# Performance work log

Measured on AMD Instinct MI355X. Metric: run time of the kernel, lower is better.

Reference implementation:

```python
import jax, jax.numpy as jnp
import numpy as np

B, LQ, LK, D = 8, 2048, 2048, 1024


def setup_inputs() -> dict:
    key = jax.random.key(0)
    k1, k2, k3, k4, k5 = jax.random.split(key, 5)
    inp = jax.random.normal(k1, (B, LQ, D), dtype=jnp.float32)
    memory = jax.random.normal(k2, (B, LK, D), dtype=jnp.float32)
    # 0/1 float mask over memory positions (1 = masked out)
    mask = (jax.random.uniform(k3, (B, LK)) < 0.15).astype(jnp.float32)
    # nn.Linear(D, 1, bias=False): weight shape [1, D], kaiming-uniform-ish init
    w_input = jax.random.uniform(k4, (1, D), dtype=jnp.float32,
                                 minval=-1.0 / np.sqrt(D), maxval=1.0 / np.sqrt(D))
    # dot_scale ~ U(0, 1/sqrt(D)) per original .uniform_(1/input_size**0.5)
    dot_scale = jax.random.uniform(k5, (D,), dtype=jnp.float32,
                                   minval=0.0, maxval=1.0 / np.sqrt(D))
    return {"input": inp, "memory": memory, "mask": mask,
            "w_input": w_input, "dot_scale": dot_scale}


def reference(input, memory, mask, w_input, dot_scale):
    # input_dot: Linear(D,1,bias=False) -> [B, Lq, 1]
    input_dot = jnp.einsum('bqd,od->bqo', input, w_input)  # o == 1
    # cross_dot: (input * dot_scale) @ memory^T -> [B, Lq, Lk]
    cross_dot = jnp.einsum('bqd,bkd->bqk', input * dot_scale, memory)
    att = input_dot + cross_dot - 1e30 * mask[:, None, :]
    weight_one = jax.nn.softmax(att, axis=-1)  # [B, Lq, Lk]
    output_one = jnp.einsum('bqk,bkd->bqd', weight_one, memory)
    return output_one
```

## Files before the change

### kernel.cpp

```cpp
#include <hip/hip_runtime.h>

#define B_  8
#define LQ_ 2048
#define LK_ 2048
#define D_  1024

typedef unsigned short u16;
using short8  = __attribute__((ext_vector_type(8))) short;
using floatx4 = __attribute__((ext_vector_type(4))) float;

#define GAS __attribute__((address_space(1)))
#define LAS __attribute__((address_space(3)))

__device__ __forceinline__ u16 f2bf(float f) {
  unsigned u = __float_as_uint(f);
  u += 0x7fffu + ((u >> 16) & 1u);
  return (u16)(u >> 16);
}
__device__ __forceinline__ float bf2f(u16 h) {
  return __uint_as_float(((unsigned)h) << 16);
}

__global__ void prep(const float* __restrict__ in, const float* __restrict__ mem,
                     const float* __restrict__ ds, u16* __restrict__ qb,
                     u16* __restrict__ mb, u16* __restrict__ mbT,
                     float* __restrict__ denom) {
  __shared__ u16 tile[64][68];
  int tid = threadIdx.x;
  int tx = tid & 15, ty = tid >> 4;
  int b = blockIdx.z;

  if (denom && blockIdx.y == 16 && blockIdx.x == 0 && blockIdx.z == 0) {
    float4 z = {0.f, 0.f, 0.f, 0.f};
    float4* d4 = (float4*)denom;
#pragma unroll
    for (int i = 0; i < (B_ * LQ_ / 4) / 256; i++)
      d4[tid + i * 256] = z;
  }

  if (blockIdx.y < 16) {
    int k0 = blockIdx.x * 64, d0 = blockIdx.y * 64;
    const float* mB = mem + (size_t)b * LK_ * D_;
    u16* mbB = mb  + (size_t)b * LK_ * D_;
    u16* mtB = mbT + (size_t)b * D_ * LK_;
#pragma unroll
    for (int i = 0; i < 4; i++) {
      int r = ty + 16 * i;
      float4 v = *(const float4*)(mB + (size_t)(k0 + r) * D_ + d0 + tx * 4);
      ushort4 h;
      h.x = f2bf(v.x); h.y = f2bf(v.y); h.z = f2bf(v.z); h.w = f2bf(v.w);
      *(ushort4*)(mbB + (size_t)(k0 + r) * D_ + d0 + tx * 4) = h;
      *(ushort4*)(&tile[r][tx * 4]) = h;
    }
    __syncthreads();
#pragma unroll
    for (int i = 0; i < 4; i++) {
      int rr = ty + 16 * i;
      ushort4 o;
      o.x = tile[tx * 4 + 0][rr];
      o.y = tile[tx * 4 + 1][rr];
      o.z = tile[tx * 4 + 2][rr];
      o.w = tile[tx * 4 + 3][rr];
      *(ushort4*)(mtB + (size_t)(d0 + rr) * LK_ + k0 + tx * 4) = o;
    }
  } else {
    int q0 = blockIdx.x * 64, d0 = (blockIdx.y - 16) * 64;
    const float* iB = in + (size_t)b * LQ_ * D_;
    u16* qB = qb + (size_t)b * LQ_ * D_;
    float4 s4 = *(const float4*)(ds + d0 + tx * 4);
#pragma unroll
    for (int i = 0; i < 4; i++) {
      int r = ty + 16 * i;
      float4 v = *(const float4*)(iB + (size_t)(q0 + r) * D_ + d0 + tx * 4);
      ushort4 h;
      h.x = f2bf(v.x * s4.x); h.y = f2bf(v.y * s4.y);
      h.z = f2bf(v.z * s4.z); h.w = f2bf(v.w * s4.w);
      *(ushort4*)(qB + (size_t)(q0 + r) * D_ + d0 + tx * 4) = h;
    }
  }
}

template <int MODE>
__global__ __launch_bounds__(512, 2) void gemm_bt(
    const u16* __restrict__ A, const u16* __restrict__ Bm,
    void* __restrict__ C, const float* __restrict__ mask,
    float* __restrict__ denom, int K, int ld, int ldc,
    size_t sA, size_t sB, size_t sC) {
  __shared__ __align__(16) u16 As[2 * 16384];
  __shared__ __align__(16) u16 Bs[2 * 16384];

  const int tid = threadIdx.x;
  const int lane = tid & 63, w = tid >> 6;
  const int lm = lane & 15, quad = (lane >> 4) & 3;
  const int wm = (w >> 2) * 128, wn = (w & 3) * 64;

  const int tiles_n = gridDim.x;
  int bid = (blockIdx.z * gridDim.y + blockIdx.y) * tiles_n + blockIdx.x;
  int bz = bid & 7;
  int s = bid >> 3;
  const int GM = 4;
  int per_group = GM * tiles_n;
  int group = s / per_group;
  int rem = s - group * per_group;
  int tm = group * GM + (rem & (GM - 1));
  int tn = rem >> 2;

  const u16* Ab = A  + (size_t)bz * sA + (size_t)(tm * 256) * ld;
  const u16* Bb = Bm + (size_t)bz * sB + (size_t)(tn * 256) * ld;

  int goff[4], lofs[4];
#pragma unroll
  for (int j = 0; j < 4; j++) {
    int c = tid + 512 * j;
    int rho = c >> 3, sl = c & 7;
    goff[j] = rho * ld + (sl ^ (rho & 7)) * 8;
    lofs[j] = c * 8;
  }

  auto stage = [&](int buf, int k0) {
#pragma unroll
    for (int j = 0; j < 4; j++)
      __builtin_amdgcn_global_load_lds((GAS void*)(Ab + goff[j] + k0),
                                       (LAS void*)(As + buf * 16384 + lofs[j]),
                                       16, 0, 0);
#pragma unroll
    for (int j = 0; j < 4; j++)
      __builtin_amdgcn_global_load_lds((GAS void*)(Bb + goff[j] + k0),
                                       (LAS void*)(Bs + buf * 16384 + lofs[j]),
                                       16, 0, 0);
  };

  const int ka0 = (((0 + quad)) ^ (lm & 7)) * 8;
  const int ka1 = (((4 + quad)) ^ (lm & 7)) * 8;

  short8 bf[8], afE[4], afO[4];
  floatx4 acc[8][4];
#pragma unroll
  for (int i = 0; i < 8; i++)
#pragma unroll
    for (int j = 0; j < 4; j++)
      acc[i][j] = {0.f, 0.f, 0.f, 0.f};
  float rs[8] = {0.f, 0.f, 0.f, 0.f, 0.f, 0.f, 0.f, 0.f};

#define SB __builtin_amdgcn_sched_barrier(0)
#define LG(N) { asm volatile("s_waitcnt lgkmcnt(" #N ")" ::: "memory"); SB; }
#define VM0   { asm volatile("s_waitcnt vmcnt(0)" ::: "memory"); SB; }

#define RD_BF(CO)                                                             \
  { _Pragma("unroll")                                                         \
    for (int n = 0; n < 4; n++) {                                             \
      bf[n * 2 + 0] = *(const short8*)(Bs + (CO) + ((wn + n * 16 + lm) << 6) + ka0); \
      bf[n * 2 + 1] = *(const short8*)(Bs + (CO) + ((wn + n * 16 + lm) << 6) + ka1); \
    } }
#define RD_AF(BANK, MP, CO)                                                   \
  { _Pragma("unroll")                                                         \
    for (int mi = 0; mi < 2; mi++) {                                          \
      BANK[mi * 2 + 0] = *(const short8*)(As + (CO) + ((wm + (MP) * 32 + mi * 16 + lm) << 6) + ka0); \
      BANK[mi * 2 + 1] = *(const short8*)(As + (CO) + ((wm + (MP) * 32 + mi * 16 + lm) << 6) + ka1); \
    } }
#define SUMS(BANK, P)                                                         \
  if constexpr (MODE == 2) {                                                  \
    _Pragma("unroll")                                                         \
    for (int mi = 0; mi < 2; mi++)                                            \
      _Pragma("unroll")                                                       \
      for (int ks = 0; ks < 2; ks++) {                                        \
        uint4 u = *(const uint4*)&BANK[mi * 2 + ks];                          \
        rs[(P) * 2 + mi] +=                                                   \
            __uint_as_float(u.x << 16) + __uint_as_float(u.x & 0xffff0000u)   \
          + __uint_as_float(u.y << 16) + __uint_as_float(u.y & 0xffff0000u)   \
          + __uint_as_float(u.z << 16) + __uint_as_float(u.z & 0xffff0000u)   \
          + __uint_as_float(u.w << 16) + __uint_as_float(u.w & 0xffff0000u);  \
      } }
#define MM(P, BANK)                                                           \
  { __builtin_amdgcn_s_setprio(1);                                            \
    _Pragma("unroll")                                                         \
    for (int mi = 0; mi < 2; mi++)                                            \
      _Pragma("unroll")                                                       \
      for (int n = 0; n < 4; n++)                                             \
        _Pragma("unroll")                                                     \
        for (int ks = 0; ks < 2; ks++)                                        \
          acc[(P) * 2 + mi][n] = __builtin_amdgcn_mfma_f32_16x16x32_bf16(     \
              BANK[mi * 2 + ks], bf[n * 2 + ks], acc[(P) * 2 + mi][n], 0, 0, 0); \
    __builtin_amdgcn_s_setprio(0); }

  const int NT = K >> 6;
  stage(0, 0);
  VM0;
  __builtin_amdgcn_s_barrier();

  for (int t = 0; t < NT; ++t) {
    const int co = (t & 1) * 16384;
    const int nbuf = (t & 1) ^ 1;
    const bool have = (t + 1 < NT);
    const int kn = (t + 1) << 6;

    SB;
    RD_BF(co) RD_AF(afE, 0, co) RD_AF(afO, 1, co) SB;
    if (have) stage(nbuf, kn);
    SB;
    LG(4)  SUMS(afE, 0) MM(0, afE) SB;
    RD_AF(afE, 2, co) SB;
    LG(4)  SUMS(afO, 1) MM(1, afO) SB;
    RD_AF(afO, 3, co) SB;
    LG(4)  SUMS(afE, 2) MM(2, afE) SB;
    LG(0)  SUMS(afO, 3) MM(3, afO) SB;
    VM0;
    __builtin_amdgcn_s_barrier();
  }
#undef MM
#undef SUMS
#undef RD_AF
#undef RD_BF
#undef LG
#undef VM0
#undef SB

  const int gm0 = tm * 256 + wm + quad * 4;
  const int gn0 = tn * 256 + wn + lm;
  const size_t cb = (size_t)bz * sC;

  if constexpr (MODE == 1) {
    const float* mrow = mask + (size_t)bz * LK_;
    bool msk[4];
#pragma unroll
    for (int ni = 0; ni < 4; ni++) msk[ni] = (mrow[gn0 + ni * 16] != 0.0f);
#pragma unroll
    for (int mi = 0; mi < 8; mi++) {
#pragma unroll
      for (int r = 0; r < 4; r++) {
        int row = gm0 + mi * 16 + r;
        size_t rowoff = cb + (size_t)row * ldc + gn0;
        float part = 0.f;
#pragma unroll
        for (int ni = 0; ni < 4; ni++) {
          float e = msk[ni] ? 0.f : __expf(acc[mi][ni][r]);
          u16 h = f2bf(e);
          ((u16*)C)[rowoff + ni * 16] = h;
          part += bf2f(h);
        }
        if (denom) {
          part += __shfl_xor(part, 1, 64);
          part += __shfl_xor(part, 2, 64);
          part += __shfl_xor(part, 4, 64);
          part += __shfl_xor(part, 8, 64);
          if (lm == 0) atomicAdd(&denom[(size_t)bz * LQ_ + row], part);
        }
      }
    }
  } else if constexpr (MODE == 0) {
#pragma unroll
    for (int mi = 0; mi < 8; mi++) {
#pragma unroll
      for (int r = 0; r < 4; r++) {
        int row = gm0 + mi * 16 + r;
        float is = 1.0f / denom[(size_t)bz * LQ_ + row];
        size_t rowoff = cb + (size_t)row * ldc + gn0;
#pragma unroll
        for (int ni = 0; ni < 4; ni++)
          ((float*)C)[rowoff + ni * 16] = acc[mi][ni][r] * is;
      }
    }
  } else {
    float inv[8];
#pragma unroll
    for (int mi = 0; mi < 8; mi++) {
      rs[mi] += __shfl_xor(rs[mi], 16, 64);
      rs[mi] += __shfl_xor(rs[mi], 32, 64);
      inv[mi] = 1.0f / rs[mi];
    }
#pragma unroll
    for (int mi = 0; mi < 8; mi++) {
#pragma unroll
      for (int r = 0; r < 4; r++) {
        size_t rowoff = cb + (size_t)(gm0 + mi * 16 + r) * ldc + gn0;
        float is = __shfl(inv[mi], quad * 4 + r, 64);
#pragma unroll
        for (int ni = 0; ni < 4; ni++)
          ((float*)C)[rowoff + ni * 16] = acc[mi][ni][r] * is;
      }
    }
  }
}

extern "C" void kernel_launch(void* const* d_in, const int* in_sizes, int n_in,
                              void* d_out, int out_size, void* d_ws, size_t ws_size,
                              hipStream_t stream) {
  const float* input  = (const float*)d_in[0];
  const float* memory = (const float*)d_in[1];
  const float* mask   = (const float*)d_in[2];
  const float* dscale = (const float*)d_in[4];

  char* ws = (char*)d_ws;
  u16* qb  = (u16*)(ws);
  u16* mb  = (u16*)(ws + (size_t)32 * 1024 * 1024);
  u16* mbT = (u16*)(ws + (size_t)64 * 1024 * 1024);
  u16* E   = (u16*)(ws + (size_t)96 * 1024 * 1024);
  size_t base = (size_t)160 * 1024 * 1024;
  bool have_denom = ws_size >= base + (size_t)B_ * LQ_ * sizeof(float);
  float* denom = have_denom ? (float*)(ws + base) : nullptr;
  float* out = (float*)d_out;

  hipLaunchKernelGGL(prep, dim3(32, 32, B_), dim3(256), 0, stream,
                     input, memory, dscale, qb, mb, mbT, denom);
  hipLaunchKernelGGL((gemm_bt<1>), dim3(LK_ / 256, LQ_ / 256, B_), dim3(512), 0,
                     stream, qb, mb, (void*)E, mask, denom, D_, D_, LK_,
                     (size_t)LQ_ * D_, (size_t)LK_ * D_, (size_t)LQ_ * LK_);
  if (have_denom)
    hipLaunchKernelGGL((gemm_bt<0>), dim3(D_ / 256, LQ_ / 256, B_), dim3(512), 0,
                       stream, E, mbT, (void*)out, nullptr, denom, LK_, LK_, D_,
                       (size_t)LQ_ * LK_, (size_t)D_ * LK_, (size_t)LQ_ * D_);
  else
    hipLaunchKernelGGL((gemm_bt<2>), dim3(D_ / 256, LQ_ / 256, B_), dim3(512), 0,
                       stream, E, mbT, (void*)out, nullptr, nullptr, LK_, LK_, D_,
                       (size_t)LQ_ * LK_, (size_t)D_ * LK_, (size_t)LQ_ * D_);
}
```

Before: 314.1 us.

## Shrink GEMM tiles to 256x128 with BK=32 and 256-thread blocks

Reworks the shared bf16 GEMM kernel to use 256x128 output tiles, a K-step of 32 and 4 waves of 256 threads instead of 256x256 tiles, K-step 64 and 8 waves. The LDS swizzle changes to a 4-slot XOR pattern. The finely interleaved LDS-read/MFMA schedule is replaced by one full fragment load, a single lgkmcnt(0) wait, then all MFMAs. This doubles the grid, lowers LDS use per block for more occupancy, and simplifies scheduling. In exchange it halves B-tile reuse, doubles the number of K iterations and barriers, and loses the overlap of LDS reads with MFMA work.

```diff
diff --git a/kernel.cpp b/kernel.cpp
--- a/kernel.cpp
+++ b/kernel.cpp
@@ -81,18 +81,18 @@
 }
 
 template <int MODE>
-__global__ __launch_bounds__(512, 2) void gemm_bt(
+__global__ __launch_bounds__(256, 2) void gemm_bt(
     const u16* __restrict__ A, const u16* __restrict__ Bm,
     void* __restrict__ C, const float* __restrict__ mask,
     float* __restrict__ denom, int K, int ld, int ldc,
     size_t sA, size_t sB, size_t sC) {
-  __shared__ __align__(16) u16 As[2 * 16384];
-  __shared__ __align__(16) u16 Bs[2 * 16384];
+  __shared__ __align__(16) u16 As[2 * 8192];
+  __shared__ __align__(16) u16 Bs[2 * 4096];
 
   const int tid = threadIdx.x;
   const int lane = tid & 63, w = tid >> 6;
   const int lm = lane & 15, quad = (lane >> 4) & 3;
-  const int wm = (w >> 2) * 128, wn = (w & 3) * 64;
+  const int wm = (w >> 1) * 128, wn = (w & 1) * 64;
 
   const int tiles_n = gridDim.x;
   int bid = (blockIdx.z * gridDim.y + blockIdx.y) * tiles_n + blockIdx.x;
@@ -106,34 +106,38 @@
   int tn = rem >> 2;
 
   const u16* Ab = A  + (size_t)bz * sA + (size_t)(tm * 256) * ld;
-  const u16* Bb = Bm + (size_t)bz * sB + (size_t)(tn * 256) * ld;
-
-  int goff[4], lofs[4];
+  const u16* Bb = Bm + (size_t)bz * sB + (size_t)(tn * 128) * ld;
+
+  int goffA[4], goffB[2];
 #pragma unroll
   for (int j = 0; j < 4; j++) {
-    int c = tid + 512 * j;
-    int rho = c >> 3, sl = c & 7;
-    goff[j] = rho * ld + (sl ^ (rho & 7)) * 8;
-    lofs[j] = c * 8;
+    int c = tid + 256 * j;
+    int rho = c >> 2, sl = c & 3;
+    goffA[j] = rho * ld + (sl ^ (rho & 3)) * 8;
+  }
+#pragma unroll
+  for (int j = 0; j < 2; j++) {
+    int c = tid + 256 * j;
+    int rho = c >> 2, sl = c & 3;
+    goffB[j] = rho * ld + (sl ^ (rho & 3)) * 8;
   }
 
   auto stage = [&](int buf, int k0) {
 #pragma unroll
     for (int j = 0; j < 4; j++)
-      __builtin_amdgcn_global_load_lds((GAS void*)(Ab + goff[j] + k0),
-                                       (LAS void*)(As + buf * 16384 + lofs[j]),
-                                       16, 0, 0);
-#pragma unroll
-    for (int j = 0; j < 4; j++)
-      __builtin_amdgcn_global_load_lds((GAS void*)(Bb + goff[j] + k0),
-                                       (LAS void*)(Bs + buf * 16384 + lofs[j]),
-                                       16, 0, 0);
+      __builtin_amdgcn_global_load_lds(
+          (GAS void*)(Ab + goffA[j] + k0),
+          (LAS void*)(As + buf * 8192 + (tid + 256 * j) * 8), 16, 0, 0);
+#pragma unroll
+    for (int j = 0; j < 2; j++)
+      __builtin_amdgcn_global_load_lds(
+          (GAS void*)(Bb + goffB[j] + k0),
+          (LAS void*)(Bs + buf * 4096 + (tid + 256 * j) * 8), 16, 0, 0);
   };
 
-  const int ka0 = (((0 + quad)) ^ (lm & 7)) * 8;
-  const int ka1 = (((4 + quad)) ^ (lm & 7)) * 8;
-
-  short8 bf[8], afE[4], afO[4];
+  const int ka = (quad ^ (lm & 3)) * 8;
+
+  short8 af[8], bf[4];
   floatx4 acc[8][4];
 #pragma unroll
   for (int i = 0; i < 8; i++)
@@ -143,80 +147,58 @@
   float rs[8] = {0.f, 0.f, 0.f, 0.f, 0.f, 0.f, 0.f, 0.f};
 
 #define SB __builtin_amdgcn_sched_barrier(0)
-#define LG(N) { asm volatile("s_waitcnt lgkmcnt(" #N ")" ::: "memory"); SB; }
-#define VM0   { asm volatile("s_waitcnt vmcnt(0)" ::: "memory"); SB; }
-
-#define RD_BF(CO)                                                             \
-  { _Pragma("unroll")                                                         \
-    for (int n = 0; n < 4; n++) {                                             \
-      bf[n * 2 + 0] = *(const short8*)(Bs + (CO) + ((wn + n * 16 + lm) << 6) + ka0); \
-      bf[n * 2 + 1] = *(const short8*)(Bs + (CO) + ((wn + n * 16 + lm) << 6) + ka1); \
-    } }
-#define RD_AF(BANK, MP, CO)                                                   \
-  { _Pragma("unroll")                                                         \
-    for (int mi = 0; mi < 2; mi++) {                                          \
-      BANK[mi * 2 + 0] = *(const short8*)(As + (CO) + ((wm + (MP) * 32 + mi * 16 + lm) << 6) + ka0); \
-      BANK[mi * 2 + 1] = *(const short8*)(As + (CO) + ((wm + (MP) * 32 + mi * 16 + lm) << 6) + ka1); \
-    } }
-#define SUMS(BANK, P)                                                         \
-  if constexpr (MODE == 2) {                                                  \
-    _Pragma("unroll")                                                         \
-    for (int mi = 0; mi < 2; mi++)                                            \
-      _Pragma("unroll")                                                       \
-      for (int ks = 0; ks < 2; ks++) {                                        \
-        uint4 u = *(const uint4*)&BANK[mi * 2 + ks];                          \
-        rs[(P) * 2 + mi] +=                                                   \
-            __uint_as_float(u.x << 16) + __uint_as_float(u.x & 0xffff0000u)   \
-          + __uint_as_float(u.y << 16) + __uint_as_float(u.y & 0xffff0000u)   \
-          + __uint_as_float(u.z << 16) + __uint_as_float(u.z & 0xffff0000u)   \
-          + __uint_as_float(u.w << 16) + __uint_as_float(u.w & 0xffff0000u);  \
-      } }
-#define MM(P, BANK)                                                           \
-  { __builtin_amdgcn_s_setprio(1);                                            \
-    _Pragma("unroll")                                                         \
-    for (int mi = 0; mi < 2; mi++)                                            \
-      _Pragma("unroll")                                                       \
-      for (int n = 0; n < 4; n++)                                             \
-        _Pragma("unroll")                                                     \
-        for (int ks = 0; ks < 2; ks++)                                        \
-          acc[(P) * 2 + mi][n] = __builtin_amdgcn_mfma_f32_16x16x32_bf16(     \
-              BANK[mi * 2 + ks], bf[n * 2 + ks], acc[(P) * 2 + mi][n], 0, 0, 0); \
-    __builtin_amdgcn_s_setprio(0); }
-
-  const int NT = K >> 6;
+#define LG0 { asm volatile("s_waitcnt lgkmcnt(0)" ::: "memory"); SB; }
+#define VM0 { asm volatile("s_waitcnt vmcnt(0)" ::: "memory"); SB; }
+
+  const int NT = K >> 5;
   stage(0, 0);
   VM0;
   __builtin_amdgcn_s_barrier();
 
   for (int t = 0; t < NT; ++t) {
-    const int co = (t & 1) * 16384;
+    const int ca = (t & 1) * 8192;
+    const int cbf = (t & 1) * 4096;
     const int nbuf = (t & 1) ^ 1;
     const bool have = (t + 1 < NT);
-    const int kn = (t + 1) << 6;
+    const int kn = (t + 1) << 5;
 
     SB;
-    RD_BF(co) RD_AF(afE, 0, co) RD_AF(afO, 1, co) SB;
+#pragma unroll
+    for (int n = 0; n < 4; n++)
+      bf[n] = *(const short8*)(Bs + cbf + ((wn + n * 16 + lm) << 5) + ka);
+#pragma unroll
+    for (int m = 0; m < 8; m++)
+      af[m] = *(const short8*)(As + ca + ((wm + m * 16 + lm) << 5) + ka);
     if (have) stage(nbuf, kn);
+    LG0;
+    if constexpr (MODE == 2) {
+#pragma unroll
+      for (int m = 0; m < 8; m++) {
+        uint4 u = *(const uint4*)&af[m];
+        rs[m] += __uint_as_float(u.x << 16) + __uint_as_float(u.x & 0xffff0000u)
+               + __uint_as_float(u.y << 16) + __uint_as_float(u.y & 0xffff0000u)
+               + __uint_as_float(u.z << 16) + __uint_as_float(u.z & 0xffff0000u)
+               + __uint_as_float(u.w << 16) + __uint_as_float(u.w & 0xffff0000u);
+      }
+    }
+    __builtin_amdgcn_s_setprio(1);
+#pragma unroll
+    for (int m = 0; m < 8; m++)
+#pragma unroll
+      for (int n = 0; n < 4; n++)
+        acc[m][n] = __builtin_amdgcn_mfma_f32_16x16x32_bf16(af[m], bf[n],
+                                                            acc[m][n], 0, 0, 0);
+    __builtin_amdgcn_s_setprio(0);
     SB;
-    LG(4)  SUMS(afE, 0) MM(0, afE) SB;
-    RD_AF(afE, 2, co) SB;
-    LG(4)  SUMS(afO, 1) MM(1, afO) SB;
-    RD_AF(afO, 3, co) SB;
-    LG(4)  SUMS(afE, 2) MM(2, afE) SB;
-    LG(0)  SUMS(afO, 3) MM(3, afO) SB;
     VM0;
     __builtin_amdgcn_s_barrier();
   }
-#undef MM
-#undef SUMS
-#undef RD_AF
-#undef RD_BF
-#undef LG
+#undef LG0
 #undef VM0
 #undef SB
 
   const int gm0 = tm * 256 + wm + quad * 4;
-  const int gn0 = tn * 256 + wn + lm;
+  const int gn0 = tn * 128 + wn + lm;
   const size_t cb = (size_t)bz * sC;
 
   if constexpr (MODE == 1) {
@@ -302,15 +284,15 @@
 
   hipLaunchKernelGGL(prep, dim3(32, 32, B_), dim3(256), 0, stream,
                      input, memory, dscale, qb, mb, mbT, denom);
-  hipLaunchKernelGGL((gemm_bt<1>), dim3(LK_ / 256, LQ_ / 256, B_), dim3(512), 0,
+  hipLaunchKernelGGL((gemm_bt<1>), dim3(LK_ / 128, LQ_ / 256, B_), dim3(256), 0,
                      stream, qb, mb, (void*)E, mask, denom, D_, D_, LK_,
                      (size_t)LQ_ * D_, (size_t)LK_ * D_, (size_t)LQ_ * LK_);
   if (have_denom)
-    hipLaunchKernelGGL((gemm_bt<0>), dim3(D_ / 256, LQ_ / 256, B_), dim3(512), 0,
+    hipLaunchKernelGGL((gemm_bt<0>), dim3(D_ / 128, LQ_ / 256, B_), dim3(256), 0,
                        stream, E, mbT, (void*)out, nullptr, denom, LK_, LK_, D_,
                        (size_t)LQ_ * LK_, (size_t)D_ * LK_, (size_t)LQ_ * D_);
   else
-    hipLaunchKernelGGL((gemm_bt<2>), dim3(D_ / 256, LQ_ / 256, B_), dim3(512), 0,
+    hipLaunchKernelGGL((gemm_bt<2>), dim3(D_ / 128, LQ_ / 256, B_), dim3(256), 0,
                        stream, E, mbT, (void*)out, nullptr, nullptr, LK_, LK_, D_,
                        (size_t)LQ_ * LK_, (size_t)D_ * LK_, (size_t)LQ_ * D_);
 }
```

Result: slower. 320.8 us (+2.1%).

## Load GEMM B operand directly from global into registers, drop B LDS tile

Applied to the files above, without the earlier changes.

The B operand fragments are now gathered straight from global memory into registers with per-lane vector loads instead of being staged through shared memory. Only A keeps the double-buffered LDS path, which halves LDS usage and removes the B LDS reads. The k-loop is restructured into two K-halves, each loading 8 A fragments before running its MFMAs. The intent is to cut LDS traffic and footprint, but it risks uncoalesced global loads and global latency exposed on the MFMA critical path, since B is reused across the 2 row-warps without LDS sharing.

```diff
diff --git a/kernel.cpp b/kernel.cpp
--- a/kernel.cpp
+++ b/kernel.cpp
@@ -87,7 +87,6 @@
     float* __restrict__ denom, int K, int ld, int ldc,
     size_t sA, size_t sB, size_t sC) {
   __shared__ __align__(16) u16 As[2 * 16384];
-  __shared__ __align__(16) u16 Bs[2 * 16384];
 
   const int tid = threadIdx.x;
   const int lane = tid & 63, w = tid >> 6;
@@ -108,32 +107,28 @@
   const u16* Ab = A  + (size_t)bz * sA + (size_t)(tm * 256) * ld;
   const u16* Bb = Bm + (size_t)bz * sB + (size_t)(tn * 256) * ld;
 
-  int goff[4], lofs[4];
+  int goff[4];
 #pragma unroll
   for (int j = 0; j < 4; j++) {
     int c = tid + 512 * j;
     int rho = c >> 3, sl = c & 7;
     goff[j] = rho * ld + (sl ^ (rho & 7)) * 8;
-    lofs[j] = c * 8;
-  }
-
-  auto stage = [&](int buf, int k0) {
+  }
+
+  auto stageA = [&](int buf, int k0) {
 #pragma unroll
     for (int j = 0; j < 4; j++)
-      __builtin_amdgcn_global_load_lds((GAS void*)(Ab + goff[j] + k0),
-                                       (LAS void*)(As + buf * 16384 + lofs[j]),
-                                       16, 0, 0);
-#pragma unroll
-    for (int j = 0; j < 4; j++)
-      __builtin_amdgcn_global_load_lds((GAS void*)(Bb + goff[j] + k0),
-                                       (LAS void*)(Bs + buf * 16384 + lofs[j]),
-                                       16, 0, 0);
+      __builtin_amdgcn_global_load_lds(
+          (GAS void*)(Ab + goff[j] + k0),
+          (LAS void*)(As + buf * 16384 + (tid + 512 * j) * 8), 16, 0, 0);
   };
 
-  const int ka0 = (((0 + quad)) ^ (lm & 7)) * 8;
-  const int ka1 = (((4 + quad)) ^ (lm & 7)) * 8;
-
-  short8 bf[8], afE[4], afO[4];
+  const int ka0 = ((0 + quad) ^ (lm & 7)) * 8;
+  const int ka1 = ((4 + quad) ^ (lm & 7)) * 8;
+
+  const u16* Bl = Bb + (size_t)(wn + lm) * ld + quad * 8;
+
+  short8 af[8], bf[8];
   floatx4 acc[8][4];
 #pragma unroll
   for (int i = 0; i < 8; i++)
@@ -143,48 +138,46 @@
   float rs[8] = {0.f, 0.f, 0.f, 0.f, 0.f, 0.f, 0.f, 0.f};
 
 #define SB __builtin_amdgcn_sched_barrier(0)
-#define LG(N) { asm volatile("s_waitcnt lgkmcnt(" #N ")" ::: "memory"); SB; }
-#define VM0   { asm volatile("s_waitcnt vmcnt(0)" ::: "memory"); SB; }
-
-#define RD_BF(CO)                                                             \
+#define LG0 { asm volatile("s_waitcnt lgkmcnt(0)" ::: "memory"); SB; }
+#define VM0 { asm volatile("s_waitcnt vmcnt(0)" ::: "memory"); SB; }
+
+#define GATH_H(KS, KT)                                                        \
   { _Pragma("unroll")                                                         \
-    for (int n = 0; n < 4; n++) {                                             \
-      bf[n * 2 + 0] = *(const short8*)(Bs + (CO) + ((wn + n * 16 + lm) << 6) + ka0); \
-      bf[n * 2 + 1] = *(const short8*)(Bs + (CO) + ((wn + n * 16 + lm) << 6) + ka1); \
-    } }
-#define RD_AF(BANK, MP, CO)                                                   \
+    for (int n = 0; n < 4; n++)                                               \
+      bf[(KS) * 4 + n] =                                                      \
+          *(const short8*)(Bl + (size_t)n * 16 * ld + (KT) + (KS) * 32); }
+#define RD_A8(KAX, CO)                                                        \
   { _Pragma("unroll")                                                         \
-    for (int mi = 0; mi < 2; mi++) {                                          \
-      BANK[mi * 2 + 0] = *(const short8*)(As + (CO) + ((wm + (MP) * 32 + mi * 16 + lm) << 6) + ka0); \
-      BANK[mi * 2 + 1] = *(const short8*)(As + (CO) + ((wm + (MP) * 32 + mi * 16 + lm) << 6) + ka1); \
-    } }
-#define SUMS(BANK, P)                                                         \
+    for (int m = 0; m < 8; m++)                                               \
+      af[m] = *(const short8*)(As + (CO) +                                    \
+          ((wm + m * 16 + lm) << 6) + (KAX)); }
+#define SUMS                                                                  \
   if constexpr (MODE == 2) {                                                  \
     _Pragma("unroll")                                                         \
-    for (int mi = 0; mi < 2; mi++)                                            \
-      _Pragma("unroll")                                                       \
-      for (int ks = 0; ks < 2; ks++) {                                        \
-        uint4 u = *(const uint4*)&BANK[mi * 2 + ks];                          \
-        rs[(P) * 2 + mi] +=                                                   \
-            __uint_as_float(u.x << 16) + __uint_as_float(u.x & 0xffff0000u)   \
-          + __uint_as_float(u.y << 16) + __uint_as_float(u.y & 0xffff0000u)   \
-          + __uint_as_float(u.z << 16) + __uint_as_float(u.z & 0xffff0000u)   \
-          + __uint_as_float(u.w << 16) + __uint_as_float(u.w & 0xffff0000u);  \
-      } }
-#define MM(P, BANK)                                                           \
+    for (int m = 0; m < 8; m++) {                                             \
+      uint4 u = *(const uint4*)&af[m];                                        \
+      rs[m] +=                                                                \
+          __uint_as_float(u.x << 16) + __uint_as_float(u.x & 0xffff0000u)     \
+        + __uint_as_float(u.y << 16) + __uint_as_float(u.y & 0xffff0000u)     \
+        + __uint_as_float(u.z << 16) + __uint_as_float(u.z & 0xffff0000u)     \
+        + __uint_as_float(u.w << 16) + __uint_as_float(u.w & 0xffff0000u);    \
+    } }
+#define MMC_K(HB)                                                             \
   { __builtin_amdgcn_s_setprio(1);                                            \
     _Pragma("unroll")                                                         \
-    for (int mi = 0; mi < 2; mi++)                                            \
+    for (int m = 0; m < 8; m++)                                               \
       _Pragma("unroll")                                                       \
       for (int n = 0; n < 4; n++)                                             \
-        _Pragma("unroll")                                                     \
-        for (int ks = 0; ks < 2; ks++)                                        \
-          acc[(P) * 2 + mi][n] = __builtin_amdgcn_mfma_f32_16x16x32_bf16(     \
-              BANK[mi * 2 + ks], bf[n * 2 + ks], acc[(P) * 2 + mi][n], 0, 0, 0); \
+        acc[m][n] = __builtin_amdgcn_mfma_f32_16x16x32_bf16(                  \
+            af[m], bf[(HB) * 4 + n], acc[m][n], 0, 0, 0);                     \
     __builtin_amdgcn_s_setprio(0); }
 
   const int NT = K >> 6;
-  stage(0, 0);
+  stageA(0, 0);
+  SB;
+  GATH_H(0, 0)
+  GATH_H(1, 0)
+  SB;
   VM0;
   __builtin_amdgcn_s_barrier();
 
@@ -195,23 +188,30 @@
     const int kn = (t + 1) << 6;
 
     SB;
-    RD_BF(co) RD_AF(afE, 0, co) RD_AF(afO, 1, co) SB;
-    if (have) stage(nbuf, kn);
-    SB;
-    LG(4)  SUMS(afE, 0) MM(0, afE) SB;
-    RD_AF(afE, 2, co) SB;
-    LG(4)  SUMS(afO, 1) MM(1, afO) SB;
-    RD_AF(afO, 3, co) SB;
-    LG(4)  SUMS(afE, 2) MM(2, afE) SB;
-    LG(0)  SUMS(afO, 3) MM(3, afO) SB;
+    if (have) stageA(nbuf, kn);
+    SB;
+    RD_A8(ka0, co)
+    SB;
+    LG0;
+    SUMS
+    MMC_K(0)
+    if (have) { GATH_H(0, kn) }
+    SB;
+    RD_A8(ka1, co)
+    SB;
+    LG0;
+    SUMS
+    MMC_K(1)
+    if (have) { GATH_H(1, kn) }
+    SB;
     VM0;
     __builtin_amdgcn_s_barrier();
   }
-#undef MM
+#undef MMC_K
 #undef SUMS
-#undef RD_AF
-#undef RD_BF
-#undef LG
+#undef RD_A8
+#undef GATH_H
+#undef LG0
 #undef VM0
 #undef SB
 
```

New measurement: 390.9 us. 24.5% more time.
